# Kernel tuning notes

Measured on AMD Instinct MI355X. Metric: run time of the kernel, lower is better.

Reference implementation:

```python
import jax, jax.numpy as jnp
import numpy as np

B, T, C, H = 2, 2048, 1024, 16
D = C // H  # 64 per-head dim


def setup_inputs() -> dict:
    key = jax.random.key(0)
    ks = jax.random.split(key, 9)
    s = 1.0 / np.sqrt(C)
    return {
        "query_src": jax.random.normal(ks[0], (B, T, C), jnp.float32),
        "key_src": jax.random.normal(ks[1], (B, T, C), jnp.float32),
        "value_src": jax.random.normal(ks[2], (B, T, C), jnp.float32),
        "Wq": jax.random.normal(ks[3], (C, C), jnp.float32) * s,
        "Wk": jax.random.normal(ks[4], (C, C), jnp.float32) * s,
        "Wv": jax.random.normal(ks[5], (C, C), jnp.float32) * s,
        "Wo": jax.random.normal(ks[6], (C, C), jnp.float32) * s,
        "bo": jax.random.normal(ks[7], (C,), jnp.float32) * s,
    }


def reference(query_src, key_src, value_src, Wq, Wk, Wv, Wo, bo):
    # Linear layers: y = x @ W.T (torch nn.Linear convention)
    q = jnp.einsum('btc,dc->btd', query_src, Wq).reshape(B, T, H, D).transpose(0, 2, 1, 3)
    k = jnp.einsum('btc,dc->btd', key_src, Wk).reshape(B, T, H, D).transpose(0, 2, 1, 3)
    v = jnp.einsum('btc,dc->btd', value_src, Wv).reshape(B, T, H, D).transpose(0, 2, 1, 3)
    # scores: [B, H, T, T]
    scores = jnp.einsum('bhqd,bhkd->bhqk', q, k)
    # FAITHFUL quirk: original divides by d**(-0.5) => multiplies by sqrt(D)
    scores = scores * jnp.sqrt(jnp.asarray(D, scores.dtype))
    # FAITHFUL quirk: softmax over dim=1 == the HEAD axis
    attn = jax.nn.softmax(scores, axis=1)
    # dropout is identity in eval mode
    out = jnp.einsum('bhqk,bhkd->bhqd', attn, v)  # [B,H,T,D]
    out = out.transpose(0, 2, 1, 3).reshape(B, T, C)
    return jnp.einsum('btc,dc->btd', out, Wo) + bo
```

## Files before the change

### kernel.cpp

```cpp
#include <hip/hip_runtime.h>
#include <cmath>

namespace {

constexpr int B_ = 2;
constexpr int T_ = 2048;
constexpr int C_ = 1024;
constexpr int H_ = 16;
constexpr int D_ = 64;

typedef _Float16 half8 __attribute__((ext_vector_type(8)));
typedef _Float16 half4 __attribute__((ext_vector_type(4)));
typedef float f32x4 __attribute__((ext_vector_type(4)));

__device__ inline f32x4 vmax4(f32x4 a, f32x4 b) {
  f32x4 r;
  r[0] = fmaxf(a[0], b[0]); r[1] = fmaxf(a[1], b[1]);
  r[2] = fmaxf(a[2], b[2]); r[3] = fmaxf(a[3], b[3]);
  return r;
}

__device__ __forceinline__ void gload16(const _Float16* g, _Float16* l) {
  __builtin_amdgcn_global_load_lds(
      (const __attribute__((address_space(1))) unsigned int*)g,
      (__attribute__((address_space(3))) unsigned int*)l, 16, 0, 0);
}

__global__ __launch_bounds__(256)
void cast7(const float* __restrict__ xq, const float* __restrict__ xk,
           const float* __restrict__ xv, const float* __restrict__ wq,
           const float* __restrict__ wk, const float* __restrict__ wv,
           const float* __restrict__ wo,
           _Float16* __restrict__ dxq, _Float16* __restrict__ dxk,
           _Float16* __restrict__ dxv, _Float16* __restrict__ dwq,
           _Float16* __restrict__ dwk, _Float16* __restrict__ dwv,
           _Float16* __restrict__ dwo) {
  constexpr size_t NX = (size_t)4 << 20;
  constexpr size_t NW = (size_t)1 << 20;
  size_t g = ((size_t)blockIdx.x * 256 + threadIdx.x) * 8;
  const float* s; _Float16* d; size_t off;
  if      (g <     NX)          { s = xq; d = dxq; off = g; }
  else if (g < 2 * NX)          { s = xk; d = dxk; off = g - NX; }
  else if (g < 3 * NX)          { s = xv; d = dxv; off = g - 2 * NX; }
  else if (g < 3 * NX + NW)     { s = wq; d = dwq; off = g - 3 * NX; }
  else if (g < 3 * NX + 2 * NW) { s = wk; d = dwk; off = g - 3 * NX - NW; }
  else if (g < 3 * NX + 3 * NW) { s = wv; d = dwv; off = g - 3 * NX - 2 * NW; }
  else                          { s = wo; d = dwo; off = g - 3 * NX - 3 * NW; }
  const float4 a = *(const float4*)(s + off);
  const float4 b = *(const float4*)(s + off + 4);
  half8 h;
  h[0] = (_Float16)a.x; h[1] = (_Float16)a.y; h[2] = (_Float16)a.z; h[3] = (_Float16)a.w;
  h[4] = (_Float16)b.x; h[5] = (_Float16)b.y; h[6] = (_Float16)b.z; h[7] = (_Float16)b.w;
  *(half8*)(d + off) = h;
}

__global__ __launch_bounds__(256, 3)
void gemm_f16nt(const _Float16* __restrict__ A0, const _Float16* __restrict__ A1,
                const _Float16* __restrict__ A2,
                const _Float16* __restrict__ W0, const _Float16* __restrict__ W1,
                const _Float16* __restrict__ W2,
                _Float16* __restrict__ Y0, _Float16* __restrict__ Y1,
                _Float16* __restrict__ Y2,
                float* __restrict__ Yf, const float* __restrict__ bias,
                int K, int N, int mode, float qsc) {
  __shared__ _Float16 sA[128 * 32];
  __shared__ _Float16 sW[128 * 32];

  const int tid  = threadIdx.x;
  const int lane = tid & 63;
  const int w    = tid >> 6;
  const int l15  = lane & 15;
  const int quad = lane >> 4;
  const int z    = blockIdx.z;
  const _Float16* A = (z == 0) ? A0 : (z == 1) ? A1 : A2;
  const _Float16* W = (z == 0) ? W0 : (z == 1) ? W1 : W2;
  _Float16*       Y = (z == 0) ? Y0 : (z == 1) ? Y1 : Y2;

  const int m0 = blockIdx.y * 128;
  const int n0 = blockIdx.x * 128;

  const int Rb  = lane >> 2;
  const int pch = lane & 3;
  const int lch = pch ^ ((Rb >> 1) & 3);
  const int swr = (l15 >> 1) & 3;

  f32x4 acc[4][4];
#pragma unroll
  for (int mt = 0; mt < 4; ++mt)
#pragma unroll
    for (int nt = 0; nt < 4; ++nt)
      acc[mt][nt] = (f32x4){0.f, 0.f, 0.f, 0.f};

  const int wm = (w >> 1) * 64;
  const int wn = (w & 1) * 64;

  for (int k0 = 0; k0 < K; k0 += 32) {
    __syncthreads();
#pragma unroll
    for (int j = 0; j < 2; ++j) {
      const int seg = w * 32 + j * 16;
      gload16(A + (size_t)(m0 + seg + Rb) * K + k0 + lch * 8, &sA[seg * 32]);
      gload16(W + (size_t)(n0 + seg + Rb) * K + k0 + lch * 8, &sW[seg * 32]);
    }
    __syncthreads();

    half8 af[4], wf[4];
#pragma unroll
    for (int mt = 0; mt < 4; ++mt) {
      const int R = wm + mt * 16 + l15;
      af[mt] = *(const half8*)&sA[R * 32 + (quad ^ swr) * 8];
    }
#pragma unroll
    for (int nt = 0; nt < 4; ++nt) {
      const int R = wn + nt * 16 + l15;
      wf[nt] = *(const half8*)&sW[R * 32 + (quad ^ swr) * 8];
    }
#pragma unroll
    for (int mt = 0; mt < 4; ++mt)
#pragma unroll
      for (int nt = 0; nt < 4; ++nt)
        acc[mt][nt] = __builtin_amdgcn_mfma_f32_16x16x32_f16(wf[nt], af[mt], acc[mt][nt], 0, 0, 0);
  }

  const float ysc = (mode == 0 && z == 0) ? qsc : 1.f;
#pragma unroll
  for (int mt = 0; mt < 4; ++mt)
#pragma unroll
    for (int nt = 0; nt < 4; ++nt) {
      const int m = m0 + wm + mt * 16 + l15;
      const int n = n0 + wn + nt * 16 + quad * 4;
      if (mode == 2) {
        float4 v;
        v.x = acc[mt][nt][0] + bias[n + 0];
        v.y = acc[mt][nt][1] + bias[n + 1];
        v.z = acc[mt][nt][2] + bias[n + 2];
        v.w = acc[mt][nt][3] + bias[n + 3];
        *(float4*)(Yf + (size_t)m * N + n) = v;
      } else {
        half4 hv;
#pragma unroll
        for (int r = 0; r < 4; ++r) hv[r] = (_Float16)(acc[mt][nt][r] * ysc);
        *(half4*)(Y + (size_t)m * N + n) = hv;
      }
    }
}

__global__ __launch_bounds__(256)
void transpose_v(const _Float16* __restrict__ Vh, _Float16* __restrict__ Vt) {
  constexpr int PAD = 1028;
  __shared__ _Float16 tile[16][PAD];
  const int b  = blockIdx.x >> 7;
  const int kt = blockIdx.x & 127;
  const int tid = threadIdx.x;

#pragma unroll
  for (int j = 0; j < 8; ++j) {
    const int ch = tid + 256 * j;
    const int t  = ch >> 7;
    const int c8 = ch & 127;
    *(half8*)&tile[t][c8 * 8] =
        *(const half8*)(Vh + ((size_t)b * T_ + kt * 16 + t) * C_ + c8 * 8);
  }
  __syncthreads();

#pragma unroll
  for (int j = 0; j < 8; ++j) {
    const int cc = tid + 256 * j;
    const int h  = cc >> 7;
    const int d  = (cc >> 1) & 63;
    const int th = (cc & 1) * 8;
    const int c  = h * 64 + d;
    half4 va, vb4;
#pragma unroll
    for (int i = 0; i < 4; ++i) va[i]  = tile[th + i][c];
#pragma unroll
    for (int i = 0; i < 4; ++i) vb4[i] = tile[th + 4 + i][c];
    const size_t base = (((size_t)b * H_ + h) * 128 + kt) * 1024 +
                        (size_t)((d & 15) * 64 + (th >> 2) * 16 + (d >> 4) * 4);
    *(half4*)(Vt + base) = va;
    *(half4*)(Vt + base + 16) = vb4;
  }
}

__global__ __launch_bounds__(256, 2)
void attn_mfma(const _Float16* __restrict__ Qhp, const _Float16* __restrict__ Khp,
               const _Float16* __restrict__ Vtp, _Float16* __restrict__ OP) {
  __shared__ f32x4 red[2][2][4][64];

  const int tid  = threadIdx.x;
  const int lane = tid & 63;
  const int w    = tid >> 6;
  const int l15  = lane & 15;
  const int quad = lane >> 4;
  const int cell = quad * 16 + l15;

  const int xcd   = blockIdx.x & 7;
  const int qi    = blockIdx.x >> 3;
  const int b     = xcd & 1;
  const int split = xcd >> 1;
  const int q0    = qi << 4;

  const size_t qrow = ((size_t)b * T_ + q0 + l15) * C_;

  half8 qh[4][2];
#pragma unroll
  for (int hl = 0; hl < 4; ++hl)
#pragma unroll
    for (int kk = 0; kk < 2; ++kk)
      qh[hl][kk] = __builtin_nontemporal_load(
          (const half8*)(Qhp + qrow + (w * 4 + hl) * 64 + kk * 32 + quad * 8));

  f32x4 oacc[4][4];
#pragma unroll
  for (int hl = 0; hl < 4; ++hl)
#pragma unroll
    for (int mt = 0; mt < 4; ++mt)
      oacc[hl][mt] = (f32x4){0.f, 0.f, 0.f, 0.f};

  const int kpb  = T_ / 4;
  const int k_lo = split * kpb;
  const int jt   = kpb / 16;

  const _Float16* vbase = Vtp + ((size_t)b * H_ + w * 4) * (128 * 1024) +
                          (size_t)(l15 * 64 + quad * 16);

  for (int j = 0; j < jt; ++j) {
    const int k0 = k_lo + j * 16;
    const int kt = k0 >> 4;
    const int p  = j & 1;
    const size_t krow = ((size_t)b * T_ + k0 + l15) * C_;

    half8 akh[4][2];
    half8 avh[4][2];
#pragma unroll
    for (int hl = 0; hl < 4; ++hl)
#pragma unroll
      for (int kk = 0; kk < 2; ++kk)
        akh[hl][kk] = *(const half8*)(Khp + krow + (w * 4 + hl) * 64 + kk * 32 + quad * 8);
#pragma unroll
    for (int hl = 0; hl < 4; ++hl) {
      const _Float16* vb = vbase + (size_t)hl * (128 * 1024) + (size_t)kt * 1024;
      avh[hl][0] = *(const half8*)(vb);
      avh[hl][1] = *(const half8*)(vb + 8);
    }

    f32x4 s[4];
#pragma unroll
    for (int hl = 0; hl < 4; ++hl) s[hl] = (f32x4){0.f, 0.f, 0.f, 0.f};
    __builtin_amdgcn_s_setprio(1);
#pragma unroll
    for (int hl = 0; hl < 4; ++hl)
#pragma unroll
      for (int kk = 0; kk < 2; ++kk)
        s[hl] = __builtin_amdgcn_mfma_f32_16x16x32_f16(akh[hl][kk], qh[hl][kk], s[hl], 0, 0, 0);
    __builtin_amdgcn_s_setprio(0);

    red[p][0][w][cell] = vmax4(vmax4(s[0], s[1]), vmax4(s[2], s[3]));
    __syncthreads();
    const f32x4 gmax = vmax4(vmax4(red[p][0][0][cell], red[p][0][1][cell]),
                             vmax4(red[p][0][2][cell], red[p][0][3][cell]));
    f32x4 ps = (f32x4){0.f, 0.f, 0.f, 0.f};
#pragma unroll
    for (int hl = 0; hl < 4; ++hl)
#pragma unroll
      for (int r = 0; r < 4; ++r) {
        const float ev = __expf(s[hl][r] - gmax[r]);
        s[hl][r] = ev;
        ps[r] += ev;
      }
    red[p][1][w][cell] = ps;
    __syncthreads();
    const f32x4 gs = red[p][1][0][cell] + red[p][1][1][cell] +
                     red[p][1][2][cell] + red[p][1][3][cell];
    f32x4 inv;
#pragma unroll
    for (int r = 0; r < 4; ++r) inv[r] = 1.f / gs[r];

    half4 pf[4];
#pragma unroll
    for (int hl = 0; hl < 4; ++hl)
#pragma unroll
      for (int r = 0; r < 4; ++r)
        pf[hl][r] = (_Float16)(s[hl][r] * inv[r]);

    __builtin_amdgcn_s_setprio(1);
#pragma unroll
    for (int hl = 0; hl < 4; ++hl) {
      const half4 v0 = __builtin_shufflevector(avh[hl][0], avh[hl][0], 0, 1, 2, 3);
      const half4 v1 = __builtin_shufflevector(avh[hl][0], avh[hl][0], 4, 5, 6, 7);
      const half4 v2 = __builtin_shufflevector(avh[hl][1], avh[hl][1], 0, 1, 2, 3);
      const half4 v3 = __builtin_shufflevector(avh[hl][1], avh[hl][1], 4, 5, 6, 7);
      oacc[hl][0] = __builtin_amdgcn_mfma_f32_16x16x16f16(v0, pf[hl], oacc[hl][0], 0, 0, 0);
      oacc[hl][1] = __builtin_amdgcn_mfma_f32_16x16x16f16(v1, pf[hl], oacc[hl][1], 0, 0, 0);
      oacc[hl][2] = __builtin_amdgcn_mfma_f32_16x16x16f16(v2, pf[hl], oacc[hl][2], 0, 0, 0);
      oacc[hl][3] = __builtin_amdgcn_mfma_f32_16x16x16f16(v3, pf[hl], oacc[hl][3], 0, 0, 0);
    }
    __builtin_amdgcn_s_setprio(0);
  }

  _Float16* op = OP + (size_t)split * ((size_t)B_ * T_ * C_);
  const size_t orow = ((size_t)b * T_ + q0 + l15) * C_;
#pragma unroll
  for (int hl = 0; hl < 4; ++hl)
#pragma unroll
    for (int mt = 0; mt < 4; ++mt) {
      half4 hv;
#pragma unroll
      for (int r = 0; r < 4; ++r) hv[r] = (_Float16)oacc[hl][mt][r];
      __builtin_nontemporal_store(
          hv, (half4*)(op + orow + (w * 4 + hl) * 64 + mt * 16 + quad * 4));
    }
}

__global__ __launch_bounds__(256)
void reduce_oh(const _Float16* __restrict__ OP, _Float16* __restrict__ AOh,
               int nsplit, size_t n) {
  const size_t i = ((size_t)blockIdx.x * 256 + threadIdx.x) * 8;
  float a[8] = {};
  for (int s = 0; s < nsplit; ++s) {
    const half8 v = *(const half8*)(OP + (size_t)s * n + i);
#pragma unroll
    for (int r = 0; r < 8; ++r) a[r] += (float)v[r];
  }
  half8 o;
#pragma unroll
  for (int r = 0; r < 8; ++r) o[r] = (_Float16)a[r];
  *(half8*)(AOh + i) = o;
}

}

extern "C" void kernel_launch(void* const* d_in, const int* in_sizes, int n_in,
                              void* d_out, int out_size, void* d_ws, size_t ws_size,
                              hipStream_t stream) {
  const float* xq = (const float*)d_in[0];
  const float* xk = (const float*)d_in[1];
  const float* xv = (const float*)d_in[2];
  const float* Wq = (const float*)d_in[3];
  const float* Wk = (const float*)d_in[4];
  const float* Wv = (const float*)d_in[5];
  const float* Wo = (const float*)d_in[6];
  const float* bo = (const float*)d_in[7];
  float* out = (float*)d_out;

  const size_t MB   = 1ull << 20;
  const size_t nBTC = (size_t)B_ * T_ * C_;

  char* wsb = (char*)d_ws;
  _Float16* Qh  = (_Float16*)(wsb + 0 * MB);
  _Float16* Kh  = (_Float16*)(wsb + 8 * MB);
  _Float16* Vt  = (_Float16*)(wsb + 16 * MB);
  _Float16* vh  = (_Float16*)(wsb + 24 * MB);
  _Float16* AOh = (_Float16*)(wsb + 24 * MB);
  _Float16* xqh = (_Float16*)(wsb + 32 * MB);
  _Float16* xkh = (_Float16*)(wsb + 40 * MB);
  _Float16* xvh = (_Float16*)(wsb + 48 * MB);
  _Float16* OP  = (_Float16*)(wsb + 32 * MB);
  _Float16* Wqh = (_Float16*)(wsb + 64 * MB);
  _Float16* Wkh = (_Float16*)(wsb + 66 * MB);
  _Float16* Wvh = (_Float16*)(wsb + 68 * MB);
  _Float16* Woh = (_Float16*)(wsb + 70 * MB);

  const int nsplit = 4;
  const int M = B_ * T_;
  dim3 blk(256);

  cast7<<<dim3(8192), blk, 0, stream>>>(xq, xk, xv, Wq, Wk, Wv, Wo,
                                        xqh, xkh, xvh, Wqh, Wkh, Wvh, Woh);

  gemm_f16nt<<<dim3(C_ / 128, M / 128, 3), blk, 0, stream>>>(
      xqh, xkh, xvh, Wqh, Wkh, Wvh, Qh, Kh, vh,
      nullptr, nullptr, C_, C_, 0, 8.f);

  transpose_v<<<dim3(B_ * 128), blk, 0, stream>>>(vh, Vt);

  attn_mfma<<<dim3(B_ * (T_ / 16) * nsplit), blk, 0, stream>>>(Qh, Kh, Vt, OP);

  reduce_oh<<<dim3((unsigned)(nBTC / 2048)), blk, 0, stream>>>(OP, AOh, nsplit, nBTC);

  gemm_f16nt<<<dim3(C_ / 128, M / 128, 1), blk, 0, stream>>>(
      AOh, nullptr, nullptr, Woh, nullptr, nullptr, nullptr, nullptr, nullptr,
      out, bo, C_, C_, 2, 1.f);
}
```

Baseline: 430.4 us.

## Stage Q tile in swizzled LDS to free registers and raise attention occupancy

```diff
diff --git a/kernel.cpp b/kernel.cpp
--- a/kernel.cpp
+++ b/kernel.cpp
@@ -182,9 +182,11 @@
   }
 }
 
-__global__ __launch_bounds__(256, 2)
+__global__ __launch_bounds__(256, 3)
 void attn_mfma(const _Float16* __restrict__ Qhp, const _Float16* __restrict__ Khp,
-               const _Float16* __restrict__ Vtp, _Float16* __restrict__ OP) {
+               const _Float16* __restrict__ Vtp, _Float16* __restrict__ OP,
+               int nsplit) {
+  __shared__ _Float16 sQ[16 * 1024];
   __shared__ f32x4 red[2][2][4][64];
 
   const int tid  = threadIdx.x;
@@ -194,21 +196,24 @@
   const int quad = lane >> 4;
   const int cell = quad * 16 + l15;
 
-  const int xcd   = blockIdx.x & 7;
-  const int qi    = blockIdx.x >> 3;
-  const int b     = xcd & 1;
-  const int split = xcd >> 1;
-  const int q0    = qi << 4;
-
-  const size_t qrow = ((size_t)b * T_ + q0 + l15) * C_;
-
-  half8 qh[4][2];
-#pragma unroll
-  for (int hl = 0; hl < 4; ++hl)
-#pragma unroll
-    for (int kk = 0; kk < 2; ++kk)
-      qh[hl][kk] = __builtin_nontemporal_load(
-          (const half8*)(Qhp + qrow + (w * 4 + hl) * 64 + kk * 32 + quad * 8));
+  const int nbq   = B_ * (T_ / 16);
+  const int split = blockIdx.x / nbq;
+  const int bq    = blockIdx.x % nbq;
+  const int b  = bq >> 7;
+  const int q0 = (bq & 127) << 4;
+
+  const _Float16* qsrc = Qhp + ((size_t)b * T_ + q0) * C_;
+#pragma unroll
+  for (int i = 0; i < 8; ++i) {
+    const int chunk = tid + 256 * i;
+    const int row   = chunk >> 7;
+    const int swz   = (chunk * 16) ^ ((row & 7) << 4);
+    *(half8*)((char*)sQ + swz) = *(const half8*)(qsrc + chunk * 8);
+  }
+  __syncthreads();
+
+  const int qlane = l15 * 2048 + quad * 16;
+  const int qxor  = (l15 & 7) << 4;
 
   f32x4 oacc[4][4];
 #pragma unroll
@@ -217,7 +222,7 @@
     for (int mt = 0; mt < 4; ++mt)
       oacc[hl][mt] = (f32x4){0.f, 0.f, 0.f, 0.f};
 
-  const int kpb  = T_ / 4;
+  const int kpb  = T_ / nsplit;
   const int k_lo = split * kpb;
   const int jt   = kpb / 16;
 
@@ -244,6 +249,14 @@
       avh[hl][1] = *(const half8*)(vb + 8);
     }
 
+    half8 qf[4][2];
+#pragma unroll
+    for (int hl = 0; hl < 4; ++hl)
+#pragma unroll
+      for (int kk = 0; kk < 2; ++kk)
+        qf[hl][kk] = *(const half8*)((const char*)sQ +
+            ((qlane + (w * 4 + hl) * 128 + kk * 64) ^ qxor));
+
     f32x4 s[4];
 #pragma unroll
     for (int hl = 0; hl < 4; ++hl) s[hl] = (f32x4){0.f, 0.f, 0.f, 0.f};
@@ -252,7 +265,7 @@
     for (int hl = 0; hl < 4; ++hl)
 #pragma unroll
       for (int kk = 0; kk < 2; ++kk)
-        s[hl] = __builtin_amdgcn_mfma_f32_16x16x32_f16(akh[hl][kk], qh[hl][kk], s[hl], 0, 0, 0);
+        s[hl] = __builtin_amdgcn_mfma_f32_16x16x32_f16(akh[hl][kk], qf[hl][kk], s[hl], 0, 0, 0);
     __builtin_amdgcn_s_setprio(0);
 
     red[p][0][w][cell] = vmax4(vmax4(s[0], s[1]), vmax4(s[2], s[3]));
@@ -274,7 +287,7 @@
                      red[p][1][2][cell] + red[p][1][3][cell];
     f32x4 inv;
 #pragma unroll
-    for (int r = 0; r < 4; ++r) inv[r] = 1.f / gs[r];
+    for (int r = 0; r < 4; ++r) inv[r] = __builtin_amdgcn_rcpf(gs[r]);
 
     half4 pf[4];
 #pragma unroll
@@ -307,8 +320,7 @@
       half4 hv;
 #pragma unroll
       for (int r = 0; r < 4; ++r) hv[r] = (_Float16)oacc[hl][mt][r];
-      __builtin_nontemporal_store(
-          hv, (half4*)(op + orow + (w * 4 + hl) * 64 + mt * 16 + quad * 4));
+      *(half4*)(op + orow + (w * 4 + hl) * 64 + mt * 16 + quad * 4) = hv;
     }
 }
 
@@ -374,7 +386,7 @@
 
   transpose_v<<<dim3(B_ * 128), blk, 0, stream>>>(vh, Vt);
 
-  attn_mfma<<<dim3(B_ * (T_ / 16) * nsplit), blk, 0, stream>>>(Qh, Kh, Vt, OP);
+  attn_mfma<<<dim3(B_ * (T_ / 16) * nsplit), blk, 0, stream>>>(Qh, Kh, Vt, OP, nsplit);
 
   reduce_oh<<<dim3((unsigned)(nBTC / 2048)), blk, 0, stream>>>(OP, AOh, nsplit, nBTC);
 
```

Result: slower. 552.6 us (+28.4%).

## Share K/V tiles across four query tiles via LDS staging in attention kernel

Applied to the files above, without the earlier changes.

```diff
diff --git a/kernel.cpp b/kernel.cpp
--- a/kernel.cpp
+++ b/kernel.cpp
@@ -24,6 +24,11 @@
   __builtin_amdgcn_global_load_lds(
       (const __attribute__((address_space(1))) unsigned int*)g,
       (__attribute__((address_space(3))) unsigned int*)l, 16, 0, 0);
+}
+
+__device__ __forceinline__ void lds_barrier() {
+  asm volatile("s_waitcnt lgkmcnt(0)" ::: "memory");
+  __builtin_amdgcn_s_barrier();
 }
 
 __global__ __launch_bounds__(256)
@@ -175,40 +180,45 @@
     for (int i = 0; i < 4; ++i) va[i]  = tile[th + i][c];
 #pragma unroll
     for (int i = 0; i < 4; ++i) vb4[i] = tile[th + 4 + i][c];
-    const size_t base = (((size_t)b * H_ + h) * 128 + kt) * 1024 +
-                        (size_t)((d & 15) * 64 + (th >> 2) * 16 + (d >> 4) * 4);
-    *(half4*)(Vt + base) = va;
-    *(half4*)(Vt + base + 16) = vb4;
+    const size_t tb = (((size_t)b * H_ + h) * 128 + kt) * 1024;
+    const int nb = ((d >> 5) & 1) * 512 + ((th >> 2) * 16 + (d & 15)) * 8 +
+                   ((d >> 4) & 1) * 4;
+    *(half4*)(Vt + tb + nb) = va;
+    *(half4*)(Vt + tb + nb + 128) = vb4;
   }
 }
 
-__global__ __launch_bounds__(256, 2)
+__global__ __launch_bounds__(1024, 4)
 void attn_mfma(const _Float16* __restrict__ Qhp, const _Float16* __restrict__ Khp,
-               const _Float16* __restrict__ Vtp, _Float16* __restrict__ OP) {
-  __shared__ f32x4 red[2][2][4][64];
+               const _Float16* __restrict__ Vtp, _Float16* __restrict__ OP,
+               int nsplit) {
+  __shared__ _Float16 sK[16 * 1024];
+  __shared__ _Float16 sV[2][16][1024];
+  __shared__ f32x4 redm[4][4][64];
+  __shared__ f32x4 reds[4][4][64];
 
   const int tid  = threadIdx.x;
   const int lane = tid & 63;
   const int w    = tid >> 6;
+  const int qt   = w >> 2;
+  const int wg   = w & 3;
   const int l15  = lane & 15;
   const int quad = lane >> 4;
   const int cell = quad * 16 + l15;
 
-  const int xcd   = blockIdx.x & 7;
-  const int qi    = blockIdx.x >> 3;
-  const int b     = xcd & 1;
-  const int split = xcd >> 1;
-  const int q0    = qi << 4;
-
-  const size_t qrow = ((size_t)b * T_ + q0 + l15) * C_;
-
+  const int nbq   = B_ * (T_ / 64);
+  const int split = blockIdx.x / nbq;
+  const int bq    = blockIdx.x % nbq;
+  const int b  = bq >> 5;
+  const int q0 = (bq & 31) << 6;
+
+  const size_t qrow = ((size_t)b * T_ + q0 + qt * 16 + l15) * C_;
   half8 qh[4][2];
 #pragma unroll
   for (int hl = 0; hl < 4; ++hl)
 #pragma unroll
     for (int kk = 0; kk < 2; ++kk)
-      qh[hl][kk] = __builtin_nontemporal_load(
-          (const half8*)(Qhp + qrow + (w * 4 + hl) * 64 + kk * 32 + quad * 8));
+      qh[hl][kk] = *(const half8*)(Qhp + qrow + (wg * 4 + hl) * 64 + kk * 32 + quad * 8);
 
   f32x4 oacc[4][4];
 #pragma unroll
@@ -217,48 +227,55 @@
     for (int mt = 0; mt < 4; ++mt)
       oacc[hl][mt] = (f32x4){0.f, 0.f, 0.f, 0.f};
 
-  const int kpb  = T_ / 4;
+  const int kpb  = T_ / nsplit;
   const int k_lo = split * kpb;
   const int jt   = kpb / 16;
 
-  const _Float16* vbase = Vtp + ((size_t)b * H_ + w * 4) * (128 * 1024) +
-                          (size_t)(l15 * 64 + quad * 16);
-
+  const int kx  = (lane * 8) ^ ((w & 7) << 3);
+  const _Float16* vhead = Vtp + ((size_t)b * H_ + w) * (128 * 1024);
+
+  auto STAGE = [&](int j) {
+    const int k0 = k_lo + j * 16;
+    const size_t kr = ((size_t)b * T_ + k0 + w) * C_;
+    gload16(Khp + kr + kx,       &sK[w * 1024]);
+    gload16(Khp + kr + 512 + kx, &sK[w * 1024 + 512]);
+    const _Float16* vsrc = vhead + (size_t)(k0 >> 4) * 1024;
+    gload16(vsrc + lane * 8,       &sV[j & 1][w][0]);
+    gload16(vsrc + lane * 8 + 512, &sV[j & 1][w][512]);
+  };
+
+  const int rsw   = (l15 & 7) << 3;
+  const int hbase = wg * 256;
+
+  STAGE(0);
   for (int j = 0; j < jt; ++j) {
-    const int k0 = k_lo + j * 16;
-    const int kt = k0 >> 4;
-    const int p  = j & 1;
-    const size_t krow = ((size_t)b * T_ + k0 + l15) * C_;
+    const int p = j & 1;
+    __syncthreads();
 
     half8 akh[4][2];
-    half8 avh[4][2];
 #pragma unroll
     for (int hl = 0; hl < 4; ++hl)
 #pragma unroll
       for (int kk = 0; kk < 2; ++kk)
-        akh[hl][kk] = *(const half8*)(Khp + krow + (w * 4 + hl) * 64 + kk * 32 + quad * 8);
-#pragma unroll
-    for (int hl = 0; hl < 4; ++hl) {
-      const _Float16* vb = vbase + (size_t)hl * (128 * 1024) + (size_t)kt * 1024;
-      avh[hl][0] = *(const half8*)(vb);
-      avh[hl][1] = *(const half8*)(vb + 8);
-    }
+        akh[hl][kk] = *(const half8*)&sK[l15 * 1024 +
+            ((hbase + hl * 64 + kk * 32 + quad * 8) ^ rsw)];
 
     f32x4 s[4];
 #pragma unroll
     for (int hl = 0; hl < 4; ++hl) s[hl] = (f32x4){0.f, 0.f, 0.f, 0.f};
-    __builtin_amdgcn_s_setprio(1);
 #pragma unroll
     for (int hl = 0; hl < 4; ++hl)
 #pragma unroll
       for (int kk = 0; kk < 2; ++kk)
         s[hl] = __builtin_amdgcn_mfma_f32_16x16x32_f16(akh[hl][kk], qh[hl][kk], s[hl], 0, 0, 0);
-    __builtin_amdgcn_s_setprio(0);
-
-    red[p][0][w][cell] = vmax4(vmax4(s[0], s[1]), vmax4(s[2], s[3]));
-    __syncthreads();
-    const f32x4 gmax = vmax4(vmax4(red[p][0][0][cell], red[p][0][1][cell]),
-                             vmax4(red[p][0][2][cell], red[p][0][3][cell]));
+
+    redm[wg][qt][cell] = vmax4(vmax4(s[0], s[1]), vmax4(s[2], s[3]));
+    lds_barrier();
+
+    if (j + 1 < jt) STAGE(j + 1);
+
+    const f32x4 gmax = vmax4(vmax4(redm[0][qt][cell], redm[1][qt][cell]),
+                             vmax4(redm[2][qt][cell], redm[3][qt][cell]));
     f32x4 ps = (f32x4){0.f, 0.f, 0.f, 0.f};
 #pragma unroll
     for (int hl = 0; hl < 4; ++hl)
@@ -268,13 +285,14 @@
         s[hl][r] = ev;
         ps[r] += ev;
       }
-    red[p][1][w][cell] = ps;
-    __syncthreads();
-    const f32x4 gs = red[p][1][0][cell] + red[p][1][1][cell] +
-                     red[p][1][2][cell] + red[p][1][3][cell];
+    reds[wg][qt][cell] = ps;
+    lds_barrier();
+
+    const f32x4 gs = reds[0][qt][cell] + reds[1][qt][cell] +
+                     reds[2][qt][cell] + reds[3][qt][cell];
     f32x4 inv;
 #pragma unroll
-    for (int r = 0; r < 4; ++r) inv[r] = 1.f / gs[r];
+    for (int r = 0; r < 4; ++r) inv[r] = __builtin_amdgcn_rcpf(gs[r]);
 
     half4 pf[4];
 #pragma unroll
@@ -283,23 +301,23 @@
       for (int r = 0; r < 4; ++r)
         pf[hl][r] = (_Float16)(s[hl][r] * inv[r]);
 
-    __builtin_amdgcn_s_setprio(1);
 #pragma unroll
     for (int hl = 0; hl < 4; ++hl) {
-      const half4 v0 = __builtin_shufflevector(avh[hl][0], avh[hl][0], 0, 1, 2, 3);
-      const half4 v1 = __builtin_shufflevector(avh[hl][0], avh[hl][0], 4, 5, 6, 7);
-      const half4 v2 = __builtin_shufflevector(avh[hl][1], avh[hl][1], 0, 1, 2, 3);
-      const half4 v3 = __builtin_shufflevector(avh[hl][1], avh[hl][1], 4, 5, 6, 7);
+      const half8 a0 = *(const half8*)&sV[p][wg * 4 + hl][cell * 8];
+      const half8 a1 = *(const half8*)&sV[p][wg * 4 + hl][cell * 8 + 512];
+      const half4 v0 = __builtin_shufflevector(a0, a0, 0, 1, 2, 3);
+      const half4 v1 = __builtin_shufflevector(a0, a0, 4, 5, 6, 7);
+      const half4 v2 = __builtin_shufflevector(a1, a1, 0, 1, 2, 3);
+      const half4 v3 = __builtin_shufflevector(a1, a1, 4, 5, 6, 7);
       oacc[hl][0] = __builtin_amdgcn_mfma_f32_16x16x16f16(v0, pf[hl], oacc[hl][0], 0, 0, 0);
       oacc[hl][1] = __builtin_amdgcn_mfma_f32_16x16x16f16(v1, pf[hl], oacc[hl][1], 0, 0, 0);
       oacc[hl][2] = __builtin_amdgcn_mfma_f32_16x16x16f16(v2, pf[hl], oacc[hl][2], 0, 0, 0);
       oacc[hl][3] = __builtin_amdgcn_mfma_f32_16x16x16f16(v3, pf[hl], oacc[hl][3], 0, 0, 0);
     }
-    __builtin_amdgcn_s_setprio(0);
   }
 
   _Float16* op = OP + (size_t)split * ((size_t)B_ * T_ * C_);
-  const size_t orow = ((size_t)b * T_ + q0 + l15) * C_;
+  const size_t orow = ((size_t)b * T_ + q0 + qt * 16 + l15) * C_;
 #pragma unroll
   for (int hl = 0; hl < 4; ++hl)
 #pragma unroll
@@ -307,8 +325,7 @@
       half4 hv;
 #pragma unroll
       for (int r = 0; r < 4; ++r) hv[r] = (_Float16)oacc[hl][mt][r];
-      __builtin_nontemporal_store(
-          hv, (half4*)(op + orow + (w * 4 + hl) * 64 + mt * 16 + quad * 4));
+      *(half4*)(op + orow + (wg * 4 + hl) * 64 + mt * 16 + quad * 4) = hv;
     }
 }
 
@@ -374,7 +391,8 @@
 
   transpose_v<<<dim3(B_ * 128), blk, 0, stream>>>(vh, Vt);
 
-  attn_mfma<<<dim3(B_ * (T_ / 16) * nsplit), blk, 0, stream>>>(Qh, Kh, Vt, OP);
+  attn_mfma<<<dim3(B_ * (T_ / 64) * nsplit), dim3(1024), 0, stream>>>(
+      Qh, Kh, Vt, OP, nsplit);
 
   reduce_oh<<<dim3((unsigned)(nBTC / 2048)), blk, 0, stream>>>(OP, AOh, nsplit, nBTC);
 
```

Result: faster. 370.9 us (-13.8%).
